# Kernel tuning notes

Measured on AMD Instinct MI355X. Metric: run time of the kernel, lower is better.

Reference implementation:

```python
import jax, jax.numpy as jnp
import numpy as np

E = 16          # num_expert
CAP = 1024


def setup_inputs() -> dict:
    key = jax.random.key(0)
    k1, k2, k3, k4 = jax.random.split(key, 4)
    B, L, D_in, D_out, S = 2, 4096, 1024, 4096, 512
    inp = jax.random.normal(k1, (B, L, D_in), jnp.float32)
    # counts must sum to B*L; use a balanced assignment (tokens pre-sorted by expert)
    fwd_expert_count = jnp.full((E,), (B * L) // E, dtype=jnp.int32)
    weight = jax.random.normal(k2, (E, D_out, D_in), jnp.float32) * (1.0 / np.sqrt(D_in))
    bias = jax.random.normal(k3, (E, D_out), jnp.float32) * 0.02
    components = jax.random.normal(k4, (E, S, D_out), jnp.float32) * (1.0 / np.sqrt(D_out))
    return {"inp": inp, "fwd_expert_count": fwd_expert_count, "weight": weight,
            "bias": bias, "components": components}


def _forward(inp, fwd_expert_count, weight, bias, components):
    flat = inp.reshape(-1, inp.shape[-1])            # [T, D_in]
    T = flat.shape[0]
    n_exp = fwd_expert_count.shape[0]
    counts = fwd_expert_count.astype(jnp.int32)
    # per-token expert id and position within its expert segment (tokens are
    # contiguous per expert, matching fastmoe's dispatch layout)
    expert_ids = jnp.repeat(jnp.arange(n_exp, dtype=jnp.int32), counts,
                            total_repeat_length=T)                    # [T]
    offsets = jnp.concatenate([jnp.zeros((1,), jnp.int32), jnp.cumsum(counts)])
    pos = jnp.arange(T, dtype=jnp.int32) - offsets[expert_ids]        # [T]
    # scatter tokens into a padded [E, CAP, D_in] buffer (static capacity)
    padded = jnp.zeros((n_exp, CAP, flat.shape[-1]), flat.dtype)
    padded = padded.at[expert_ids, pos].set(flat)
    # grouped expert GEMM: y_e = x_e @ W_e^T + b_e  (padded rows never read back)
    y = jnp.einsum('eci,eoi->eco', padded, weight) + bias[:, None, :]  # [E, CAP, D_out]
    # projection onto components (einsum 'nkd,ksd->nks' in padded layout)
    proj = jnp.einsum('ecd,esd->ecs', y, components)                   # [E, CAP, S]
    # gather real tokens back (the upscale_proj branch in the source is dead code:
    # its result is never used in the returned output)
    out = proj[expert_ids, pos]                                        # [T, S]
    return out.reshape(inp.shape[:-1] + (proj.shape[-1],))


def reference(inp, fwd_expert_count, weight, bias, components):
    return _forward(inp, fwd_expert_count, weight, bias, components)
```

## Files before the change

### kernel.cpp

```cpp
#include <hip/hip_runtime.h>


#define NEXP 16
#define TTOK 8192
#define DIN  1024
#define DOUT 4096
#define SDIM 512
#define LDSS 40

typedef short short8 __attribute__((ext_vector_type(8)));
typedef float floatx4 __attribute__((ext_vector_type(4)));
typedef unsigned short ushort_t;

__device__ __forceinline__ ushort_t f2bf(float f) {
    union { float f; unsigned u; } v; v.f = f;
    unsigned r = v.u + 0x7FFFu + ((v.u >> 16) & 1u);
    return (ushort_t)(r >> 16);
}

#define GLL16(g, l) __builtin_amdgcn_global_load_lds( \
    (const __attribute__((address_space(1))) void*)(g), \
    (__attribute__((address_space(3))) void*)(l), 16, 0, 0)

__global__ __launch_bounds__(256)
void cvt_kernel(const float* __restrict__ src, ushort_t* __restrict__ dst, int n8) {
    const int i = blockIdx.x * 256 + threadIdx.x;
    if (i >= n8) return;
    const float4 a = ((const float4*)src)[2 * i];
    const float4 b = ((const float4*)src)[2 * i + 1];
    short8 o;
    o[0] = (short)f2bf(a.x); o[1] = (short)f2bf(a.y);
    o[2] = (short)f2bf(a.z); o[3] = (short)f2bf(a.w);
    o[4] = (short)f2bf(b.x); o[5] = (short)f2bf(b.y);
    o[6] = (short)f2bf(b.z); o[7] = (short)f2bf(b.w);
    ((short8*)dst)[i] = o;
}

__global__ __launch_bounds__(256, 3)
void gemm1_f(const ushort_t* __restrict__ Xb, const int* __restrict__ counts,
             const ushort_t* __restrict__ Wb, const float* __restrict__ bias,
             ushort_t* __restrict__ Y) {
    __shared__ __align__(16) ushort_t As[128 * 32];
    __shared__ __align__(16) ushort_t Bs[128 * 32];

    const int l = ((blockIdx.x & 7) << 8) | (blockIdx.x >> 3);
    const int e = l >> 7;
    const int r = l & 127;
    const int n_tile = r >> 2, m_tile = r & 3;

    int off = 0;
    for (int i = 0; i < e; ++i) off += counts[i];
    const int cnt = counts[e];

    const int t = threadIdx.x, wave = t >> 6, lane = t & 63;
    const int wm = (wave & 1) << 6, wn = (wave >> 1) << 6;
    const int l15 = lane & 15, quad = lane >> 4;

    const int g = (lane & 3) ^ ((lane >> 3) & 3);
    const int c0 = wave * 2, c1 = wave * 2 + 1;
    const int ar0 = c0 * 16 + (lane >> 2), ar1 = c1 * 16 + (lane >> 2);
    int xr0 = off + (m_tile << 7) + ar0; if (xr0 >= TTOK) xr0 = TTOK - 1;
    int xr1 = off + (m_tile << 7) + ar1; if (xr1 >= TTOK) xr1 = TTOK - 1;
    const ushort_t* gA0 = Xb + (size_t)xr0 * DIN + g * 8;
    const ushort_t* gA1 = Xb + (size_t)xr1 * DIN + g * 8;
    const ushort_t* Wp = Wb + (size_t)e * DOUT * DIN + (size_t)(n_tile << 7) * DIN;
    const ushort_t* gB0 = Wp + (size_t)ar0 * DIN + g * 8;
    const ushort_t* gB1 = Wp + (size_t)ar1 * DIN + g * 8;
    ushort_t* lA0 = As + c0 * 512; ushort_t* lA1 = As + c1 * 512;
    ushort_t* lB0 = Bs + c0 * 512; ushort_t* lB1 = Bs + c1 * 512;

    const int sw = (quad ^ ((l15 >> 1) & 3)) << 3;

    floatx4 acc[4][4] = {};

    for (int k0 = 0; k0 < DIN; k0 += 32) {
        GLL16(gA0, lA0); GLL16(gA1, lA1);
        GLL16(gB0, lB0); GLL16(gB1, lB1);
        gA0 += 32; gA1 += 32; gB0 += 32; gB1 += 32;
        __syncthreads();
        short8 af[4], bfr[4];
        #pragma unroll
        for (int i = 0; i < 4; ++i) {
            af[i]  = *(const short8*)&As[(wm + (i << 4) + l15) * 32 + sw];
            bfr[i] = *(const short8*)&Bs[(wn + (i << 4) + l15) * 32 + sw];
        }
        #pragma unroll
        for (int mi = 0; mi < 4; ++mi)
            #pragma unroll
            for (int ni = 0; ni < 4; ++ni)
                acc[mi][ni] = __builtin_amdgcn_mfma_f32_16x16x32_bf16(
                    af[mi], bfr[ni], acc[mi][ni], 0, 0, 0);
        __syncthreads();
    }

    float bv[4];
    #pragma unroll
    for (int ni = 0; ni < 4; ++ni)
        bv[ni] = bias[e * DOUT + (n_tile << 7) + wn + (ni << 4) + l15];

    #pragma unroll
    for (int mi = 0; mi < 4; ++mi) {
        #pragma unroll
        for (int rg = 0; rg < 4; ++rg) {
            const int trow = (m_tile << 7) + wm + (mi << 4) + (quad << 2) + rg;
            if (trow < cnt) {
                ushort_t* yp = Y + (size_t)(off + trow) * DOUT + (n_tile << 7) + wn;
                #pragma unroll
                for (int ni = 0; ni < 4; ++ni)
                    yp[(ni << 4) + l15] = f2bf(acc[mi][ni][rg] + bv[ni]);
            }
        }
    }
}

__global__ __launch_bounds__(256, 3)
void gemm2_f(const ushort_t* __restrict__ Y, const int* __restrict__ counts,
             const ushort_t* __restrict__ Cb, float* __restrict__ P) {
    __shared__ __align__(16) ushort_t As[128 * 32];
    __shared__ __align__(16) ushort_t Bs[128 * 32];

    const int l = ((blockIdx.x & 7) << 6) | (blockIdx.x >> 3);
    const int e = l >> 5;
    const int r = l & 31;
    const int n_tile = r >> 3;
    const int kh = (r >> 2) & 1;
    const int m_tile = r & 3;

    int off = 0;
    for (int i = 0; i < e; ++i) off += counts[i];
    const int cnt = counts[e];

    const int t = threadIdx.x, wave = t >> 6, lane = t & 63;
    const int wm = (wave & 1) << 6, wn = (wave >> 1) << 6;
    const int l15 = lane & 15, quad = lane >> 4;

    const int g = (lane & 3) ^ ((lane >> 3) & 3);
    const int c0 = wave * 2, c1 = wave * 2 + 1;
    const int ar0 = c0 * 16 + (lane >> 2), ar1 = c1 * 16 + (lane >> 2);
    int yr0 = off + (m_tile << 7) + ar0; if (yr0 >= TTOK) yr0 = TTOK - 1;
    int yr1 = off + (m_tile << 7) + ar1; if (yr1 >= TTOK) yr1 = TTOK - 1;
    const int kbase = kh * 2048;
    const ushort_t* gA0 = Y + (size_t)yr0 * DOUT + kbase + g * 8;
    const ushort_t* gA1 = Y + (size_t)yr1 * DOUT + kbase + g * 8;
    const ushort_t* Cp = Cb + (size_t)e * SDIM * DOUT + (size_t)(n_tile << 7) * DOUT;
    const ushort_t* gB0 = Cp + (size_t)ar0 * DOUT + kbase + g * 8;
    const ushort_t* gB1 = Cp + (size_t)ar1 * DOUT + kbase + g * 8;
    ushort_t* lA0 = As + c0 * 512; ushort_t* lA1 = As + c1 * 512;
    ushort_t* lB0 = Bs + c0 * 512; ushort_t* lB1 = Bs + c1 * 512;

    const int sw = (quad ^ ((l15 >> 1) & 3)) << 3;

    floatx4 acc[4][4] = {};

    for (int it = 0; it < 64; ++it) {
        GLL16(gA0, lA0); GLL16(gA1, lA1);
        GLL16(gB0, lB0); GLL16(gB1, lB1);
        gA0 += 32; gA1 += 32; gB0 += 32; gB1 += 32;
        __syncthreads();
        short8 af[4], bfr[4];
        #pragma unroll
        for (int i = 0; i < 4; ++i) {
            af[i]  = *(const short8*)&As[(wm + (i << 4) + l15) * 32 + sw];
            bfr[i] = *(const short8*)&Bs[(wn + (i << 4) + l15) * 32 + sw];
        }
        #pragma unroll
        for (int mi = 0; mi < 4; ++mi)
            #pragma unroll
            for (int ni = 0; ni < 4; ++ni)
                acc[mi][ni] = __builtin_amdgcn_mfma_f32_16x16x32_bf16(
                    af[mi], bfr[ni], acc[mi][ni], 0, 0, 0);
        __syncthreads();
    }

    float* Pk = P + (size_t)kh * (TTOK * SDIM);
    #pragma unroll
    for (int mi = 0; mi < 4; ++mi) {
        #pragma unroll
        for (int rg = 0; rg < 4; ++rg) {
            const int trow = (m_tile << 7) + wm + (mi << 4) + (quad << 2) + rg;
            if (trow < cnt) {
                float* op = Pk + (size_t)(off + trow) * SDIM + (n_tile << 7) + wn;
                #pragma unroll
                for (int ni = 0; ni < 4; ++ni)
                    op[(ni << 4) + l15] = acc[mi][ni][rg];
            }
        }
    }
}

__global__ __launch_bounds__(256)
void reduce2_kernel(const float* __restrict__ P, float* __restrict__ O) {
    const int i = blockIdx.x * 256 + threadIdx.x;
    const float4 a = ((const float4*)P)[i];
    const float4 b = ((const float4*)(P + (size_t)TTOK * SDIM))[i];
    ((float4*)O)[i] = make_float4(a.x + b.x, a.y + b.y, a.z + b.z, a.w + b.w);
}

__global__ __launch_bounds__(256, 2)
void gemm1_o(const float* __restrict__ X, const int* __restrict__ counts,
             const float* __restrict__ W, const float* __restrict__ bias,
             ushort_t* __restrict__ Y) {
    __shared__ __align__(16) ushort_t As[128 * LDSS];
    __shared__ __align__(16) ushort_t Bs[128 * LDSS];
    const int bid = blockIdx.x;
    const int e = bid >> 7, r_ = bid & 127;
    const int n_tile = r_ >> 2, m_tile = r_ & 3;
    int off = 0;
    for (int i = 0; i < e; ++i) off += counts[i];
    const int cnt = counts[e];
    const int t = threadIdx.x, wave = t >> 6, lane = t & 63;
    const int wm = (wave & 1) << 6, wn = (wave >> 1) << 6;
    const int l15 = lane & 15, quad = lane >> 4;
    const float* Wp = W + (size_t)e * DOUT * DIN + (size_t)(n_tile << 7) * DIN;
    floatx4 acc[4][4] = {};
    const int srow = t >> 3, scol = (t & 7) << 2;
    for (int k0 = 0; k0 < DIN; k0 += 32) {
        #pragma unroll
        for (int p = 0; p < 4; ++p) {
            const int row = srow + (p << 5);
            int grow = off + (m_tile << 7) + row;
            if (grow >= TTOK) grow = 0;
            const float4 v = *(const float4*)(X + (size_t)grow * DIN + k0 + scol);
            unsigned lo = (unsigned)f2bf(v.x) | ((unsigned)f2bf(v.y) << 16);
            unsigned hi = (unsigned)f2bf(v.z) | ((unsigned)f2bf(v.w) << 16);
            *(uint2*)&As[row * LDSS + scol] = make_uint2(lo, hi);
        }
        #pragma unroll
        for (int p = 0; p < 4; ++p) {
            const int row = srow + (p << 5);
            const float4 v = *(const float4*)(Wp + (size_t)row * DIN + k0 + scol);
            unsigned lo = (unsigned)f2bf(v.x) | ((unsigned)f2bf(v.y) << 16);
            unsigned hi = (unsigned)f2bf(v.z) | ((unsigned)f2bf(v.w) << 16);
            *(uint2*)&Bs[row * LDSS + scol] = make_uint2(lo, hi);
        }
        __syncthreads();
        short8 af[4], bfr[4];
        #pragma unroll
        for (int i = 0; i < 4; ++i) {
            af[i]  = *(const short8*)&As[(wm + (i << 4) + l15) * LDSS + (quad << 3)];
            bfr[i] = *(const short8*)&Bs[(wn + (i << 4) + l15) * LDSS + (quad << 3)];
        }
        #pragma unroll
        for (int mi = 0; mi < 4; ++mi)
            #pragma unroll
            for (int ni = 0; ni < 4; ++ni)
                acc[mi][ni] = __builtin_amdgcn_mfma_f32_16x16x32_bf16(
                    af[mi], bfr[ni], acc[mi][ni], 0, 0, 0);
        __syncthreads();
    }
    float bv[4];
    #pragma unroll
    for (int ni = 0; ni < 4; ++ni)
        bv[ni] = bias[e * DOUT + (n_tile << 7) + wn + (ni << 4) + l15];
    #pragma unroll
    for (int mi = 0; mi < 4; ++mi)
        #pragma unroll
        for (int rg = 0; rg < 4; ++rg) {
            const int trow = (m_tile << 7) + wm + (mi << 4) + (quad << 2) + rg;
            if (trow < cnt) {
                ushort_t* yp = Y + (size_t)(off + trow) * DOUT + (n_tile << 7) + wn;
                #pragma unroll
                for (int ni = 0; ni < 4; ++ni)
                    yp[(ni << 4) + l15] = f2bf(acc[mi][ni][rg] + bv[ni]);
            }
        }
}

__global__ __launch_bounds__(256, 2)
void gemm2_o(const ushort_t* __restrict__ Y, const int* __restrict__ counts,
             const float* __restrict__ C, float* __restrict__ O) {
    __shared__ __align__(16) ushort_t As[128 * LDSS];
    __shared__ __align__(16) ushort_t Bs[128 * LDSS];
    const int bid = blockIdx.x;
    const int e = bid >> 4, r_ = bid & 15;
    const int n_tile = r_ >> 2, m_tile = r_ & 3;
    int off = 0;
    for (int i = 0; i < e; ++i) off += counts[i];
    const int cnt = counts[e];
    const int t = threadIdx.x, wave = t >> 6, lane = t & 63;
    const int wm = (wave & 1) << 6, wn = (wave >> 1) << 6;
    const int l15 = lane & 15, quad = lane >> 4;
    const float* Cp = C + (size_t)e * SDIM * DOUT + (size_t)(n_tile << 7) * DOUT;
    floatx4 acc[4][4] = {};
    const int arow = t >> 2, achk = (t & 3) << 3;
    const int srow = t >> 3, scol = (t & 7) << 2;
    for (int k0 = 0; k0 < DOUT; k0 += 32) {
        #pragma unroll
        for (int p = 0; p < 2; ++p) {
            const int row = arow + (p << 6);
            int grow = off + (m_tile << 7) + row;
            if (grow >= TTOK) grow = 0;
            const short8 v = *(const short8*)(Y + (size_t)grow * DOUT + k0 + achk);
            *(short8*)&As[row * LDSS + achk] = v;
        }
        #pragma unroll
        for (int p = 0; p < 4; ++p) {
            const int row = srow + (p << 5);
            const float4 v = *(const float4*)(Cp + (size_t)row * DOUT + k0 + scol);
            unsigned lo = (unsigned)f2bf(v.x) | ((unsigned)f2bf(v.y) << 16);
            unsigned hi = (unsigned)f2bf(v.z) | ((unsigned)f2bf(v.w) << 16);
            *(uint2*)&Bs[row * LDSS + scol] = make_uint2(lo, hi);
        }
        __syncthreads();
        short8 af[4], bfr[4];
        #pragma unroll
        for (int i = 0; i < 4; ++i) {
            af[i]  = *(const short8*)&As[(wm + (i << 4) + l15) * LDSS + (quad << 3)];
            bfr[i] = *(const short8*)&Bs[(wn + (i << 4) + l15) * LDSS + (quad << 3)];
        }
        #pragma unroll
        for (int mi = 0; mi < 4; ++mi)
            #pragma unroll
            for (int ni = 0; ni < 4; ++ni)
                acc[mi][ni] = __builtin_amdgcn_mfma_f32_16x16x32_bf16(
                    af[mi], bfr[ni], acc[mi][ni], 0, 0, 0);
        __syncthreads();
    }
    #pragma unroll
    for (int mi = 0; mi < 4; ++mi)
        #pragma unroll
        for (int rg = 0; rg < 4; ++rg) {
            const int trow = (m_tile << 7) + wm + (mi << 4) + (quad << 2) + rg;
            if (trow < cnt) {
                float* op = O + (size_t)(off + trow) * SDIM + (n_tile << 7) + wn;
                #pragma unroll
                for (int ni = 0; ni < 4; ++ni)
                    op[(ni << 4) + l15] = acc[mi][ni][rg];
            }
        }
}

extern "C" void kernel_launch(void* const* d_in, const int* in_sizes, int n_in,
                              void* d_out, int out_size, void* d_ws, size_t ws_size,
                              hipStream_t stream) {
    const float* X      = (const float*)d_in[0];
    const int*   counts = (const int*)d_in[1];
    const float* W      = (const float*)d_in[2];
    const float* bias   = (const float*)d_in[3];
    const float* comp   = (const float*)d_in[4];
    float* out = (float*)d_out;

    const size_t OFF_XB = 0;
    const size_t OFF_WB = 16777216;
    const size_t OFF_CB = 150994944;
    const size_t OFF_Y  = 218103808;
    const size_t NEED   = 285212672;

    if (ws_size >= NEED) {
        ushort_t* Xb = (ushort_t*)((char*)d_ws + OFF_XB);
        ushort_t* Wb = (ushort_t*)((char*)d_ws + OFF_WB);
        ushort_t* Cb = (ushort_t*)((char*)d_ws + OFF_CB);
        ushort_t* Y  = (ushort_t*)((char*)d_ws + OFF_Y);
        float*    P  = (float*)d_ws;

        cvt_kernel<<<dim3(4096),  dim3(256), 0, stream>>>(X, Xb, 1048576);
        cvt_kernel<<<dim3(32768), dim3(256), 0, stream>>>(W, Wb, 8388608);
        cvt_kernel<<<dim3(16384), dim3(256), 0, stream>>>(comp, Cb, 4194304);
        gemm1_f<<<dim3(2048), dim3(256), 0, stream>>>(Xb, counts, Wb, bias, Y);
        gemm2_f<<<dim3(512),  dim3(256), 0, stream>>>(Y, counts, Cb, P);
        reduce2_kernel<<<dim3(4096), dim3(256), 0, stream>>>(P, out);
    } else {
        ushort_t* Y = (ushort_t*)d_ws;
        gemm1_o<<<dim3(2048), dim3(256), 0, stream>>>(X, counts, W, bias, Y);
        gemm2_o<<<dim3(256),  dim3(256), 0, stream>>>(Y, counts, comp, out);
    }
}
```

Measured before the change: 654.9 us.

## Stage gemm1 epilogue through LDS and split gemm2 K into four slices

The gemm1 epilogue now writes bias-added bf16 results into shared memory in two halves, then stores them as coalesced 16-byte vectors to Y instead of scattered 2-byte stores. gemm2 splits K into four slices instead of two, doubling the block count to improve CU occupancy, and the reduction kernel sums four partial buffers. This trades extra partial-sum memory traffic and additional syncs for better store coalescing and parallelism.

```diff
diff --git a/kernel.cpp b/kernel.cpp
--- a/kernel.cpp
+++ b/kernel.cpp
@@ -7,6 +7,7 @@
 #define DOUT 4096
 #define SDIM 512
 #define LDSS 40
+#define RPS  132
 
 typedef short short8 __attribute__((ext_vector_type(8)));
 typedef float floatx4 __attribute__((ext_vector_type(4)));
@@ -40,8 +41,9 @@
 void gemm1_f(const ushort_t* __restrict__ Xb, const int* __restrict__ counts,
              const ushort_t* __restrict__ Wb, const float* __restrict__ bias,
              ushort_t* __restrict__ Y) {
-    __shared__ __align__(16) ushort_t As[128 * 32];
-    __shared__ __align__(16) ushort_t Bs[128 * 32];
+    __shared__ __align__(16) ushort_t smem[8448];
+    ushort_t* As = smem;
+    ushort_t* Bs = smem + 4096;
 
     const int l = ((blockIdx.x & 7) << 8) | (blockIdx.x >> 3);
     const int e = l >> 7;
@@ -98,17 +100,32 @@
     for (int ni = 0; ni < 4; ++ni)
         bv[ni] = bias[e * DOUT + (n_tile << 7) + wn + (ni << 4) + l15];
 
-    #pragma unroll
-    for (int mi = 0; mi < 4; ++mi) {
-        #pragma unroll
-        for (int rg = 0; rg < 4; ++rg) {
-            const int trow = (m_tile << 7) + wm + (mi << 4) + (quad << 2) + rg;
-            if (trow < cnt) {
-                ushort_t* yp = Y + (size_t)(off + trow) * DOUT + (n_tile << 7) + wn;
+    const int hsel = wm >> 6;
+    #pragma unroll
+    for (int h = 0; h < 2; ++h) {
+        __syncthreads();
+        if (hsel == h) {
+            #pragma unroll
+            for (int mi = 0; mi < 4; ++mi)
                 #pragma unroll
                 for (int ni = 0; ni < 4; ++ni)
-                    yp[(ni << 4) + l15] = f2bf(acc[mi][ni][rg] + bv[ni]);
-            }
+                    #pragma unroll
+                    for (int rg = 0; rg < 4; ++rg) {
+                        const int rr = (mi << 4) + (quad << 2) + rg;
+                        smem[rr * RPS + wn + (ni << 4) + l15] =
+                            f2bf(acc[mi][ni][rg] + bv[ni]);
+                    }
+        }
+        __syncthreads();
+        #pragma unroll
+        for (int p = 0; p < 4; ++p) {
+            const int chunk = (p << 8) + t;
+            const int rr = chunk >> 4;
+            const int cc = (chunk & 15) << 3;
+            const int lrow = (m_tile << 7) + (h << 6) + rr;
+            if (lrow < cnt)
+                *(short8*)(Y + (size_t)(off + lrow) * DOUT + (n_tile << 7) + cc)
+                    = *(const short8*)&smem[rr * RPS + cc];
         }
     }
 }
@@ -116,14 +133,15 @@
 __global__ __launch_bounds__(256, 3)
 void gemm2_f(const ushort_t* __restrict__ Y, const int* __restrict__ counts,
              const ushort_t* __restrict__ Cb, float* __restrict__ P) {
-    __shared__ __align__(16) ushort_t As[128 * 32];
-    __shared__ __align__(16) ushort_t Bs[128 * 32];
-
-    const int l = ((blockIdx.x & 7) << 6) | (blockIdx.x >> 3);
-    const int e = l >> 5;
-    const int r = l & 31;
-    const int n_tile = r >> 3;
-    const int kh = (r >> 2) & 1;
+    __shared__ __align__(16) ushort_t smem[8192];
+    ushort_t* As = smem;
+    ushort_t* Bs = smem + 4096;
+
+    const int l = ((blockIdx.x & 7) << 7) | (blockIdx.x >> 3);
+    const int e = l >> 6;
+    const int r = l & 63;
+    const int kslice = r >> 4;
+    const int n_tile = (r >> 2) & 3;
     const int m_tile = r & 3;
 
     int off = 0;
@@ -139,7 +157,7 @@
     const int ar0 = c0 * 16 + (lane >> 2), ar1 = c1 * 16 + (lane >> 2);
     int yr0 = off + (m_tile << 7) + ar0; if (yr0 >= TTOK) yr0 = TTOK - 1;
     int yr1 = off + (m_tile << 7) + ar1; if (yr1 >= TTOK) yr1 = TTOK - 1;
-    const int kbase = kh * 2048;
+    const int kbase = kslice << 10;
     const ushort_t* gA0 = Y + (size_t)yr0 * DOUT + kbase + g * 8;
     const ushort_t* gA1 = Y + (size_t)yr1 * DOUT + kbase + g * 8;
     const ushort_t* Cp = Cb + (size_t)e * SDIM * DOUT + (size_t)(n_tile << 7) * DOUT;
@@ -152,7 +170,7 @@
 
     floatx4 acc[4][4] = {};
 
-    for (int it = 0; it < 64; ++it) {
+    for (int it = 0; it < 32; ++it) {
         GLL16(gA0, lA0); GLL16(gA1, lA1);
         GLL16(gB0, lB0); GLL16(gB1, lB1);
         gA0 += 32; gA1 += 32; gB0 += 32; gB1 += 32;
@@ -172,7 +190,7 @@
         __syncthreads();
     }
 
-    float* Pk = P + (size_t)kh * (TTOK * SDIM);
+    float* Pk = P + (size_t)kslice * (TTOK * SDIM);
     #pragma unroll
     for (int mi = 0; mi < 4; ++mi) {
         #pragma unroll
@@ -189,11 +207,15 @@
 }
 
 __global__ __launch_bounds__(256)
-void reduce2_kernel(const float* __restrict__ P, float* __restrict__ O) {
+void reduce4_kernel(const float* __restrict__ P, float* __restrict__ O) {
+    const size_t S1 = (size_t)TTOK * SDIM / 4;
     const int i = blockIdx.x * 256 + threadIdx.x;
     const float4 a = ((const float4*)P)[i];
-    const float4 b = ((const float4*)(P + (size_t)TTOK * SDIM))[i];
-    ((float4*)O)[i] = make_float4(a.x + b.x, a.y + b.y, a.z + b.z, a.w + b.w);
+    const float4 b = ((const float4*)P)[i + S1];
+    const float4 c = ((const float4*)P)[i + 2 * S1];
+    const float4 d = ((const float4*)P)[i + 3 * S1];
+    ((float4*)O)[i] = make_float4(a.x + b.x + c.x + d.x, a.y + b.y + c.y + d.y,
+                                  a.z + b.z + c.z + d.z, a.w + b.w + c.w + d.w);
 }
 
 __global__ __launch_bounds__(256, 2)
@@ -340,14 +362,13 @@
     const float* comp   = (const float*)d_in[4];
     float* out = (float*)d_out;
 
-    const size_t OFF_XB = 0;
     const size_t OFF_WB = 16777216;
     const size_t OFF_CB = 150994944;
     const size_t OFF_Y  = 218103808;
     const size_t NEED   = 285212672;
 
     if (ws_size >= NEED) {
-        ushort_t* Xb = (ushort_t*)((char*)d_ws + OFF_XB);
+        ushort_t* Xb = (ushort_t*)d_ws;
         ushort_t* Wb = (ushort_t*)((char*)d_ws + OFF_WB);
         ushort_t* Cb = (ushort_t*)((char*)d_ws + OFF_CB);
         ushort_t* Y  = (ushort_t*)((char*)d_ws + OFF_Y);
@@ -357,8 +378,8 @@
         cvt_kernel<<<dim3(32768), dim3(256), 0, stream>>>(W, Wb, 8388608);
         cvt_kernel<<<dim3(16384), dim3(256), 0, stream>>>(comp, Cb, 4194304);
         gemm1_f<<<dim3(2048), dim3(256), 0, stream>>>(Xb, counts, Wb, bias, Y);
-        gemm2_f<<<dim3(512),  dim3(256), 0, stream>>>(Y, counts, Cb, P);
-        reduce2_kernel<<<dim3(4096), dim3(256), 0, stream>>>(P, out);
+        gemm2_f<<<dim3(1024), dim3(256), 0, stream>>>(Y, counts, Cb, P);
+        reduce4_kernel<<<dim3(4096), dim3(256), 0, stream>>>(P, out);
     } else {
         ushort_t* Y = (ushort_t*)d_ws;
         gemm1_o<<<dim3(2048), dim3(256), 0, stream>>>(X, counts, W, bias, Y);
```

Result: no change. 657.6 us (+0.4%).
